# Kernel tuning notes

Measured on AMD Instinct MI355X. Metric: run time of the kernel, lower is better.

## Reference

```python
import jax, jax.numpy as jnp
import numpy as np

B, C, KC, H, W, M = 8, 512, 256, 128, 128, 19


def _cbr(x, Wt, s, b):
    # 1x1 conv (no bias) + folded BatchNorm affine + ReLU.  x: [B,Cin,H,W], Wt: [Cout,Cin]
    y = jnp.einsum('oc,bchw->bohw', Wt, x)
    return jax.nn.relu(y * s[None, :, None, None] + b[None, :, None, None])


def setup_inputs() -> dict:
    key = jax.random.key(0)
    ks = jax.random.split(key, 10)
    inp = {
        'x': jax.random.normal(ks[0], (B, C, H, W), jnp.float32),
        'proxy': jax.random.normal(ks[1], (B, C, M, 1), jnp.float32),
    }
    # fan-in scaled weights so activations stay O(1)
    inp['W_p1'] = jax.random.normal(ks[2], (KC, C), jnp.float32) * (C ** -0.5)
    inp['W_p2'] = jax.random.normal(ks[3], (KC, KC), jnp.float32) * (KC ** -0.5)
    inp['W_o1'] = jax.random.normal(ks[4], (KC, C), jnp.float32) * (C ** -0.5)
    inp['W_o2'] = jax.random.normal(ks[5], (KC, KC), jnp.float32) * (KC ** -0.5)
    inp['W_d1'] = jax.random.normal(ks[6], (KC, C), jnp.float32) * (C ** -0.5)
    inp['W_d2'] = jax.random.normal(ks[7], (KC, KC), jnp.float32) * (KC ** -0.5)
    inp['W_u'] = jax.random.normal(ks[8], (C, KC), jnp.float32) * (KC ** -0.5)
    for name, dim in [('p1', KC), ('p2', KC), ('o1', KC), ('o2', KC), ('d1', KC), ('d2', KC), ('u', C)]:
        inp['s_' + name] = jnp.ones((dim,), jnp.float32)
        inp['b_' + name] = jnp.zeros((dim,), jnp.float32)
    return inp


def reference(x, proxy, W_p1, s_p1, b_p1, W_p2, s_p2, b_p2,
              W_o1, s_o1, b_o1, W_o2, s_o2, b_o2,
              W_d1, s_d1, b_d1, W_d2, s_d2, b_d2,
              W_u, s_u, b_u):
    b, _, h, w = x.shape
    kc = W_p1.shape[0]
    # pixel query / object key / object value projections (two ConvBnRelu each)
    q = _cbr(_cbr(x, W_p1, s_p1, b_p1), W_p2, s_p2, b_p2)          # [B,KC,H,W]
    k = _cbr(_cbr(proxy, W_o1, s_o1, b_o1), W_o2, s_o2, b_o2)      # [B,KC,M,1]
    v = _cbr(_cbr(proxy, W_d1, s_d1, b_d1), W_d2, s_d2, b_d2)      # [B,KC,M,1]
    q = q.reshape(b, kc, h * w)                                    # [B,KC,P]
    k = k.reshape(b, kc, -1)                                       # [B,KC,M]
    v = v.reshape(b, kc, -1)                                       # [B,KC,M]
    sim = jnp.einsum('bkp,bkm->bpm', q, k) * (kc ** -0.5)          # [B,P,M]
    sim = jax.nn.softmax(sim, axis=-1)
    ctx = jnp.einsum('bpm,bkm->bkp', sim, v).reshape(b, kc, h, w)  # [B,KC,H,W]
    return _cbr(ctx, W_u, s_u, b_u)                                # [B,C,H,W]
```

## Files before the change

### kernel.cpp

```cpp
#include <hip/hip_runtime.h>
#include <hip/hip_bf16.h>
#include <cstddef>

constexpr int B_  = 8;
constexpr int C_  = 512;
constexpr int KC_ = 256;
constexpr int M_  = 19;
constexpr int P_  = 128 * 128;

typedef short frag8 __attribute__((ext_vector_type(8)));
typedef float f32x4 __attribute__((ext_vector_type(4)));

__device__ __forceinline__ unsigned pk_bf16(float a, float b) {
    union { __hip_bfloat162 h; unsigned u; } cv;
    cv.h = __float22bfloat162_rn(make_float2(a, b));
    return cv.u;
}
__device__ __forceinline__ ushort bf16_1(float a) {
    union { __hip_bfloat16 h; ushort u; } cv;
    cv.h = __float2bfloat16(a);
    return cv.u;
}

__device__ __forceinline__ void two_stage_proj(
    const float* __restrict__ pS, float* __restrict__ t1,
    const float* __restrict__ W1, const float* __restrict__ s1, const float* __restrict__ b1,
    const float* __restrict__ W2, const float* __restrict__ s2, const float* __restrict__ b2,
    float* __restrict__ outg, int b, int tid)
{
    float acc[M_];
#pragma unroll
    for (int m = 0; m < M_; ++m) acc[m] = 0.f;
    const float4* wrow = reinterpret_cast<const float4*>(W1 + (size_t)tid * C_);
    for (int c4 = 0; c4 < C_ / 4; ++c4) {
        float4 w = wrow[c4];
        const float* pr = pS + c4 * 4 * M_;
#pragma unroll
        for (int m = 0; m < M_; ++m) acc[m] = fmaf(w.x, pr[m], acc[m]);
#pragma unroll
        for (int m = 0; m < M_; ++m) acc[m] = fmaf(w.y, pr[M_ + m], acc[m]);
#pragma unroll
        for (int m = 0; m < M_; ++m) acc[m] = fmaf(w.z, pr[2 * M_ + m], acc[m]);
#pragma unroll
        for (int m = 0; m < M_; ++m) acc[m] = fmaf(w.w, pr[3 * M_ + m], acc[m]);
    }
    float s = s1[tid], bb = b1[tid];
    __syncthreads();
#pragma unroll
    for (int m = 0; m < M_; ++m) t1[tid * M_ + m] = fmaxf(fmaf(acc[m], s, bb), 0.f);
    __syncthreads();
#pragma unroll
    for (int m = 0; m < M_; ++m) acc[m] = 0.f;
    const float4* wrow2 = reinterpret_cast<const float4*>(W2 + (size_t)tid * KC_);
    for (int c4 = 0; c4 < KC_ / 4; ++c4) {
        float4 w = wrow2[c4];
        const float* tr = t1 + c4 * 4 * M_;
#pragma unroll
        for (int m = 0; m < M_; ++m) acc[m] = fmaf(w.x, tr[m], acc[m]);
#pragma unroll
        for (int m = 0; m < M_; ++m) acc[m] = fmaf(w.y, tr[M_ + m], acc[m]);
#pragma unroll
        for (int m = 0; m < M_; ++m) acc[m] = fmaf(w.z, tr[2 * M_ + m], acc[m]);
#pragma unroll
        for (int m = 0; m < M_; ++m) acc[m] = fmaf(w.w, tr[3 * M_ + m], acc[m]);
    }
    s = s2[tid]; bb = b2[tid];
#pragma unroll
    for (int m = 0; m < M_; ++m)
        outg[((size_t)b * KC_ + tid) * M_ + m] = fmaxf(fmaf(acc[m], s, bb), 0.f);
}

__global__ __launch_bounds__(256) void kv_kernel(
    const float* __restrict__ proxy,
    const float* __restrict__ Wo1, const float* __restrict__ so1, const float* __restrict__ bo1,
    const float* __restrict__ Wo2, const float* __restrict__ so2, const float* __restrict__ bo2,
    const float* __restrict__ Wd1, const float* __restrict__ sd1, const float* __restrict__ bd1,
    const float* __restrict__ Wd2, const float* __restrict__ sd2, const float* __restrict__ bd2,
    float* __restrict__ Kg, float* __restrict__ Vg)
{
    __shared__ float pS[C_ * M_];
    __shared__ float t1[KC_ * M_];
    const int b = blockIdx.x, tid = threadIdx.x;
    for (int i = tid; i < C_ * M_; i += 256) pS[i] = proxy[(size_t)b * C_ * M_ + i];
    __syncthreads();
    two_stage_proj(pS, t1, Wo1, so1, bo1, Wo2, so2, bo2, Kg, b, tid);
    __syncthreads();
    two_stage_proj(pS, t1, Wd1, sd1, bd1, Wd2, sd2, bd2, Vg, b, tid);
}

template <int K, bool IN_F32, bool OUT_F32>
__global__ __launch_bounds__(256) void mfma_cbr(
    const float* __restrict__ W, const void* __restrict__ Xv,
    const float* __restrict__ sc, const float* __restrict__ bi,
    void* __restrict__ Yv, int O)
{
    __shared__ ushort As[128][40];
    __shared__ ushort Bs[128][40];

    const int tid = threadIdx.x;
    const int m0 = blockIdx.x * 128;
    const int n0 = blockIdx.y * 128;
    const int b  = blockIdx.z;
    const int wave = tid >> 6, lane = tid & 63;
    const int quad = lane >> 4, l15 = lane & 15;
    const int mq = (wave & 1) * 64, nq = (wave >> 1) * 64;

    const int am  = tid >> 1;
    const int akh = (tid & 1) * 16;
    const int pp  = (tid & 63) * 2;
    const int bkg = (tid >> 6) * 8;

    const float*  Wp = W + (size_t)(m0 + am) * K + akh;
    const float*  Xf = (const float*)Xv  + (size_t)b * K * P_ + n0 + pp;
    const ushort* Xh = (const ushort*)Xv + (size_t)b * K * P_ + n0 + pp;

    f32x4 acc[4][4];
#pragma unroll
    for (int i = 0; i < 4; ++i)
#pragma unroll
        for (int j = 0; j < 4; ++j) acc[i][j] = {0.f, 0.f, 0.f, 0.f};

    for (int k0 = 0; k0 < K; k0 += 32) {
        float4 wa0 = *(const float4*)(Wp + k0);
        float4 wa1 = *(const float4*)(Wp + k0 + 4);
        float4 wa2 = *(const float4*)(Wp + k0 + 8);
        float4 wa3 = *(const float4*)(Wp + k0 + 12);
        unsigned bd0[4], bd1[4];
        if constexpr (IN_F32) {
            float2 xr[8];
#pragma unroll
            for (int j = 0; j < 8; ++j)
                xr[j] = *(const float2*)(Xf + (size_t)(k0 + bkg + j) * P_);
#pragma unroll
            for (int i = 0; i < 4; ++i) {
                bd0[i] = pk_bf16(xr[2 * i].x, xr[2 * i + 1].x);
                bd1[i] = pk_bf16(xr[2 * i].y, xr[2 * i + 1].y);
            }
        } else {
            unsigned xr[8];
#pragma unroll
            for (int j = 0; j < 8; ++j)
                xr[j] = *(const unsigned*)(Xh + (size_t)(k0 + bkg + j) * P_);
#pragma unroll
            for (int i = 0; i < 4; ++i) {
                bd0[i] = (xr[2 * i] & 0xffffu) | (xr[2 * i + 1] << 16);
                bd1[i] = (xr[2 * i] >> 16)    | (xr[2 * i + 1] & 0xffff0000u);
            }
        }
        unsigned ad0[4] = { pk_bf16(wa0.x, wa0.y), pk_bf16(wa0.z, wa0.w),
                            pk_bf16(wa1.x, wa1.y), pk_bf16(wa1.z, wa1.w) };
        unsigned ad1[4] = { pk_bf16(wa2.x, wa2.y), pk_bf16(wa2.z, wa2.w),
                            pk_bf16(wa3.x, wa3.y), pk_bf16(wa3.z, wa3.w) };

        __syncthreads();
        *(int4*)(&As[am][akh])     = *(int4*)ad0;
        *(int4*)(&As[am][akh + 8]) = *(int4*)ad1;
        *(int4*)(&Bs[pp][bkg])     = *(int4*)bd0;
        *(int4*)(&Bs[pp + 1][bkg]) = *(int4*)bd1;
        __syncthreads();

        frag8 af[4], bfv[4];
#pragma unroll
        for (int f = 0; f < 4; ++f) {
            af[f]  = *(const frag8*)(&As[mq + f * 16 + l15][quad * 8]);
            bfv[f] = *(const frag8*)(&Bs[nq + f * 16 + l15][quad * 8]);
        }
#pragma unroll
        for (int i = 0; i < 4; ++i)
#pragma unroll
            for (int j = 0; j < 4; ++j)
                acc[i][j] = __builtin_amdgcn_mfma_f32_16x16x32_bf16(
                    af[i], bfv[j], acc[i][j], 0, 0, 0);
    }

#pragma unroll
    for (int i = 0; i < 4; ++i) {
        const int ob = m0 + mq + i * 16 + quad * 4;
        float s[4], bbv[4];
#pragma unroll
        for (int r = 0; r < 4; ++r) { s[r] = sc[ob + r]; bbv[r] = bi[ob + r]; }
#pragma unroll
        for (int j = 0; j < 4; ++j) {
            const int p = n0 + nq + j * 16 + l15;
#pragma unroll
            for (int r = 0; r < 4; ++r) {
                float v = fmaxf(fmaf(acc[i][j][r], s[r], bbv[r]), 0.f);
                if constexpr (OUT_F32)
                    ((float*)Yv)[((size_t)b * O + ob + r) * P_ + p] = v;
                else
                    ((ushort*)Yv)[((size_t)b * O + ob + r) * P_ + p] = bf16_1(v);
            }
        }
    }
}

__global__ __launch_bounds__(256) void attn_kernel(
    ushort* __restrict__ Q,
    const float* __restrict__ Kg, const float* __restrict__ Vg)
{
    __shared__ float kS[KC_ * M_];
    __shared__ float vS[KC_ * M_];
    const int b = blockIdx.y;
    const int p = (blockIdx.x * 256 + threadIdx.x) * 2;
    for (int i = threadIdx.x; i < KC_ * M_; i += 256) {
        kS[i] = Kg[(size_t)b * KC_ * M_ + i];
        vS[i] = Vg[(size_t)b * KC_ * M_ + i];
    }
    __syncthreads();

    float s0[M_], s1[M_];
#pragma unroll
    for (int m = 0; m < M_; ++m) { s0[m] = 0.f; s1[m] = 0.f; }

    unsigned* Qb = reinterpret_cast<unsigned*>(Q + (size_t)b * KC_ * P_ + p);
    for (int kc = 0; kc < KC_; ++kc) {
        unsigned u = Qb[(size_t)kc * (P_ / 2)];
        float qa = __uint_as_float(u << 16);
        float qb = __uint_as_float(u & 0xffff0000u);
        const float* kr = kS + kc * M_;
#pragma unroll
        for (int m = 0; m < M_; ++m) {
            s0[m] = fmaf(qa, kr[m], s0[m]);
            s1[m] = fmaf(qb, kr[m], s1[m]);
        }
    }

    float mx0 = -1e30f, mx1 = -1e30f;
#pragma unroll
    for (int m = 0; m < M_; ++m) {
        s0[m] *= 0.0625f; s1[m] *= 0.0625f;
        mx0 = fmaxf(mx0, s0[m]); mx1 = fmaxf(mx1, s1[m]);
    }
    float sum0 = 0.f, sum1 = 0.f;
#pragma unroll
    for (int m = 0; m < M_; ++m) {
        s0[m] = __expf(s0[m] - mx0); sum0 += s0[m];
        s1[m] = __expf(s1[m] - mx1); sum1 += s1[m];
    }
    const float i0 = 1.f / sum0, i1 = 1.f / sum1;
#pragma unroll
    for (int m = 0; m < M_; ++m) { s0[m] *= i0; s1[m] *= i1; }

    for (int kc = 0; kc < KC_; ++kc) {
        const float* vr = vS + kc * M_;
        float a0 = 0.f, a1 = 0.f;
#pragma unroll
        for (int m = 0; m < M_; ++m) {
            a0 = fmaf(s0[m], vr[m], a0);
            a1 = fmaf(s1[m], vr[m], a1);
        }
        Qb[(size_t)kc * (P_ / 2)] = pk_bf16(a0, a1);
    }
}

extern "C" void kernel_launch(void* const* d_in, const int* in_sizes, int n_in,
                              void* d_out, int out_size, void* d_ws, size_t ws_size,
                              hipStream_t stream)
{
    const float* x     = (const float*)d_in[0];
    const float* proxy = (const float*)d_in[1];
    const float* W_p1  = (const float*)d_in[2];
    const float* W_p2  = (const float*)d_in[3];
    const float* W_o1  = (const float*)d_in[4];
    const float* W_o2  = (const float*)d_in[5];
    const float* W_d1  = (const float*)d_in[6];
    const float* W_d2  = (const float*)d_in[7];
    const float* W_u   = (const float*)d_in[8];
    const float* s_p1  = (const float*)d_in[9];  const float* b_p1 = (const float*)d_in[10];
    const float* s_p2  = (const float*)d_in[11]; const float* b_p2 = (const float*)d_in[12];
    const float* s_o1  = (const float*)d_in[13]; const float* b_o1 = (const float*)d_in[14];
    const float* s_o2  = (const float*)d_in[15]; const float* b_o2 = (const float*)d_in[16];
    const float* s_d1  = (const float*)d_in[17]; const float* b_d1 = (const float*)d_in[18];
    const float* s_d2  = (const float*)d_in[19]; const float* b_d2 = (const float*)d_in[20];
    const float* s_u   = (const float*)d_in[21]; const float* b_u  = (const float*)d_in[22];

    float* out = (float*)d_out;
    float* Kg  = out;
    float* Vg  = Kg + (size_t)B_ * KC_ * M_;
    ushort* q1 = (ushort*)d_ws;
    ushort* q2 = q1 + (size_t)B_ * KC_ * P_;

    kv_kernel<<<dim3(B_), dim3(256), 0, stream>>>(
        proxy, W_o1, s_o1, b_o1, W_o2, s_o2, b_o2,
               W_d1, s_d1, b_d1, W_d2, s_d2, b_d2, Kg, Vg);

    mfma_cbr<C_, true, false><<<dim3(KC_ / 128, P_ / 128, B_), dim3(256), 0, stream>>>(
        W_p1, x, s_p1, b_p1, q1, KC_);

    mfma_cbr<KC_, false, false><<<dim3(KC_ / 128, P_ / 128, B_), dim3(256), 0, stream>>>(
        W_p2, q1, s_p2, b_p2, q2, KC_);

    attn_kernel<<<dim3(P_ / 512, B_), dim3(256), 0, stream>>>(q2, Kg, Vg);

    mfma_cbr<KC_, false, true><<<dim3(C_ / 128, P_ / 128, B_), dim3(256), 0, stream>>>(
        W_u, q2, s_u, b_u, out, C_);
}
```

Measured before the change: 888.7 us.

## Switch intermediates to pixel-major bf16, pre-convert weights, and double-buffer GEMMs via direct LDS loads

Intermediate activations are now stored pixel-major (channel contiguous), so the bf16-input GEMMs can load rows with 16-byte global_load_lds into double-buffered, XOR-swizzled LDS tiles. Weights are converted to bf16 once in a front kernel that also splits the K and V projections across more blocks. Grid indices are swizzled for cache locality. The attention kernel now reads and writes one pixel per thread with vectorized 8-element channel loads. The aim is fewer redundant weight conversions, wider and coalesced loads, and overlap of loads with MFMA. The cost is more workspace and layout complexity.

```diff
diff --git a/kernel.cpp b/kernel.cpp
--- a/kernel.cpp
+++ b/kernel.cpp
@@ -1,6 +1,7 @@
 #include <hip/hip_runtime.h>
 #include <hip/hip_bf16.h>
 #include <cstddef>
+#include <cstdint>
 
 constexpr int B_  = 8;
 constexpr int C_  = 512;
@@ -10,6 +11,7 @@
 
 typedef short frag8 __attribute__((ext_vector_type(8)));
 typedef float f32x4 __attribute__((ext_vector_type(4)));
+typedef unsigned short u16x8 __attribute__((ext_vector_type(8)));
 
 __device__ __forceinline__ unsigned pk_bf16(float a, float b) {
     union { __hip_bfloat162 h; unsigned u; } cv;
@@ -20,6 +22,15 @@
     union { __hip_bfloat16 h; ushort u; } cv;
     cv.h = __float2bfloat16(a);
     return cv.u;
+}
+__device__ __forceinline__ float bf16_f(ushort u) {
+    return __uint_as_float(((unsigned)u) << 16);
+}
+
+__device__ __forceinline__ void gll16(const ushort* g, ushort* l) {
+    __builtin_amdgcn_global_load_lds(
+        (__attribute__((address_space(1))) void*)(ushort*)g,
+        (__attribute__((address_space(3))) void*)l, 16, 0, 0);
 }
 
 __device__ __forceinline__ void two_stage_proj(
@@ -70,37 +81,62 @@
         outg[((size_t)b * KC_ + tid) * M_ + m] = fmaxf(fmaf(acc[m], s, bb), 0.f);
 }
 
-__global__ __launch_bounds__(256) void kv_kernel(
+__device__ __forceinline__ void cvt_w(const float* __restrict__ s, ushort* __restrict__ d,
+                                      int n4, int cid, int nb) {
+    for (int i = cid * 256 + (int)threadIdx.x; i < n4; i += nb * 256) {
+        float4 f = ((const float4*)s)[i];
+        ushort4 h;
+        h.x = bf16_1(f.x); h.y = bf16_1(f.y); h.z = bf16_1(f.z); h.w = bf16_1(f.w);
+        ((ushort4*)d)[i] = h;
+    }
+}
+
+__global__ __launch_bounds__(256) void front_kernel(
     const float* __restrict__ proxy,
     const float* __restrict__ Wo1, const float* __restrict__ so1, const float* __restrict__ bo1,
     const float* __restrict__ Wo2, const float* __restrict__ so2, const float* __restrict__ bo2,
     const float* __restrict__ Wd1, const float* __restrict__ sd1, const float* __restrict__ bd1,
     const float* __restrict__ Wd2, const float* __restrict__ sd2, const float* __restrict__ bd2,
-    float* __restrict__ Kg, float* __restrict__ Vg)
+    float* __restrict__ Kg, float* __restrict__ Vg,
+    const float* __restrict__ Wp1f, const float* __restrict__ Wp2f, const float* __restrict__ Wuf,
+    ushort* __restrict__ Wp1b, ushort* __restrict__ Wp2b, ushort* __restrict__ Wub)
 {
     __shared__ float pS[C_ * M_];
     __shared__ float t1[KC_ * M_];
-    const int b = blockIdx.x, tid = threadIdx.x;
-    for (int i = tid; i < C_ * M_; i += 256) pS[i] = proxy[(size_t)b * C_ * M_ + i];
-    __syncthreads();
-    two_stage_proj(pS, t1, Wo1, so1, bo1, Wo2, so2, bo2, Kg, b, tid);
-    __syncthreads();
-    two_stage_proj(pS, t1, Wd1, sd1, bd1, Wd2, sd2, bd2, Vg, b, tid);
-}
-
-template <int K, bool IN_F32, bool OUT_F32>
-__global__ __launch_bounds__(256) void mfma_cbr(
-    const float* __restrict__ W, const void* __restrict__ Xv,
+    const int bx = blockIdx.x, tid = threadIdx.x;
+    if (bx < 16) {
+        const int b = bx >> 1;
+        for (int i = tid; i < C_ * M_; i += 256) pS[i] = proxy[(size_t)b * C_ * M_ + i];
+        __syncthreads();
+        if (bx & 1)
+            two_stage_proj(pS, t1, Wd1, sd1, bd1, Wd2, sd2, bd2, Vg, b, tid);
+        else
+            two_stage_proj(pS, t1, Wo1, so1, bo1, Wo2, so2, bo2, Kg, b, tid);
+    } else {
+        const int cid = bx - 16, nb = (int)gridDim.x - 16;
+        cvt_w(Wp1f, Wp1b, KC_ * C_ / 4, cid, nb);
+        cvt_w(Wp2f, Wp2b, KC_ * KC_ / 4, cid, nb);
+        cvt_w(Wuf,  Wub,  C_ * KC_ / 4, cid, nb);
+    }
+}
+
+__global__ __launch_bounds__(256) void cbr_f32in(
+    const ushort* __restrict__ Wb, const float* __restrict__ X,
     const float* __restrict__ sc, const float* __restrict__ bi,
-    void* __restrict__ Yv, int O)
-{
-    __shared__ ushort As[128][40];
-    __shared__ ushort Bs[128][40];
+    ushort* __restrict__ Y)
+{
+    constexpr int K = C_;
+    constexpr int O = KC_;
+    __shared__ __align__(16) ushort As[128][40];
+    __shared__ __align__(16) ushort Bs[128][40];
 
     const int tid = threadIdx.x;
-    const int m0 = blockIdx.x * 128;
-    const int n0 = blockIdx.y * 128;
-    const int b  = blockIdx.z;
+    const unsigned bid = blockIdx.x;
+    const unsigned swz = (bid & 7) * (gridDim.x >> 3) + (bid >> 3);
+    const int m0 = (int)(swz & 1) * 128;
+    const int n0 = (int)((swz >> 1) & 127) * 128;
+    const int b  = (int)(swz >> 8);
+
     const int wave = tid >> 6, lane = tid & 63;
     const int quad = lane >> 4, l15 = lane & 15;
     const int mq = (wave & 1) * 64, nq = (wave >> 1) * 64;
@@ -110,9 +146,8 @@
     const int pp  = (tid & 63) * 2;
     const int bkg = (tid >> 6) * 8;
 
-    const float*  Wp = W + (size_t)(m0 + am) * K + akh;
-    const float*  Xf = (const float*)Xv  + (size_t)b * K * P_ + n0 + pp;
-    const ushort* Xh = (const ushort*)Xv + (size_t)b * K * P_ + n0 + pp;
+    const ushort* Wp = Wb + (size_t)(m0 + am) * K + akh;
+    const float*  Xf = X + (size_t)b * K * P_ + n0 + pp;
 
     f32x4 acc[4][4];
 #pragma unroll
@@ -121,42 +156,24 @@
         for (int j = 0; j < 4; ++j) acc[i][j] = {0.f, 0.f, 0.f, 0.f};
 
     for (int k0 = 0; k0 < K; k0 += 32) {
-        float4 wa0 = *(const float4*)(Wp + k0);
-        float4 wa1 = *(const float4*)(Wp + k0 + 4);
-        float4 wa2 = *(const float4*)(Wp + k0 + 8);
-        float4 wa3 = *(const float4*)(Wp + k0 + 12);
+        u16x8 wa0 = *(const u16x8*)(Wp + k0);
+        u16x8 wa1 = *(const u16x8*)(Wp + k0 + 8);
+        float2 xr[8];
+#pragma unroll
+        for (int j = 0; j < 8; ++j)
+            xr[j] = *(const float2*)(Xf + (size_t)(k0 + bkg + j) * P_);
         unsigned bd0[4], bd1[4];
-        if constexpr (IN_F32) {
-            float2 xr[8];
-#pragma unroll
-            for (int j = 0; j < 8; ++j)
-                xr[j] = *(const float2*)(Xf + (size_t)(k0 + bkg + j) * P_);
-#pragma unroll
-            for (int i = 0; i < 4; ++i) {
-                bd0[i] = pk_bf16(xr[2 * i].x, xr[2 * i + 1].x);
-                bd1[i] = pk_bf16(xr[2 * i].y, xr[2 * i + 1].y);
-            }
-        } else {
-            unsigned xr[8];
-#pragma unroll
-            for (int j = 0; j < 8; ++j)
-                xr[j] = *(const unsigned*)(Xh + (size_t)(k0 + bkg + j) * P_);
-#pragma unroll
-            for (int i = 0; i < 4; ++i) {
-                bd0[i] = (xr[2 * i] & 0xffffu) | (xr[2 * i + 1] << 16);
-                bd1[i] = (xr[2 * i] >> 16)    | (xr[2 * i + 1] & 0xffff0000u);
-            }
-        }
-        unsigned ad0[4] = { pk_bf16(wa0.x, wa0.y), pk_bf16(wa0.z, wa0.w),
-                            pk_bf16(wa1.x, wa1.y), pk_bf16(wa1.z, wa1.w) };
-        unsigned ad1[4] = { pk_bf16(wa2.x, wa2.y), pk_bf16(wa2.z, wa2.w),
-                            pk_bf16(wa3.x, wa3.y), pk_bf16(wa3.z, wa3.w) };
+#pragma unroll
+        for (int i = 0; i < 4; ++i) {
+            bd0[i] = pk_bf16(xr[2 * i].x, xr[2 * i + 1].x);
+            bd1[i] = pk_bf16(xr[2 * i].y, xr[2 * i + 1].y);
+        }
 
         __syncthreads();
-        *(int4*)(&As[am][akh])     = *(int4*)ad0;
-        *(int4*)(&As[am][akh + 8]) = *(int4*)ad1;
-        *(int4*)(&Bs[pp][bkg])     = *(int4*)bd0;
-        *(int4*)(&Bs[pp + 1][bkg]) = *(int4*)bd1;
+        *(u16x8*)(&As[am][akh])     = wa0;
+        *(u16x8*)(&As[am][akh + 8]) = wa1;
+        *(int4*)(&Bs[pp][bkg])      = *(int4*)bd0;
+        *(int4*)(&Bs[pp + 1][bkg])  = *(int4*)bd1;
         __syncthreads();
 
         frag8 af[4], bfv[4];
@@ -175,81 +192,170 @@
 
 #pragma unroll
     for (int i = 0; i < 4; ++i) {
-        const int ob = m0 + mq + i * 16 + quad * 4;
-        float s[4], bbv[4];
-#pragma unroll
-        for (int r = 0; r < 4; ++r) { s[r] = sc[ob + r]; bbv[r] = bi[ob + r]; }
+        const int o0 = m0 + mq + i * 16 + quad * 4;
+        float s4[4], b4[4];
+#pragma unroll
+        for (int r = 0; r < 4; ++r) { s4[r] = sc[o0 + r]; b4[r] = bi[o0 + r]; }
 #pragma unroll
         for (int j = 0; j < 4; ++j) {
             const int p = n0 + nq + j * 16 + l15;
-#pragma unroll
-            for (int r = 0; r < 4; ++r) {
-                float v = fmaxf(fmaf(acc[i][j][r], s[r], bbv[r]), 0.f);
-                if constexpr (OUT_F32)
-                    ((float*)Yv)[((size_t)b * O + ob + r) * P_ + p] = v;
-                else
-                    ((ushort*)Yv)[((size_t)b * O + ob + r) * P_ + p] = bf16_1(v);
+            float v0 = fmaxf(fmaf(acc[i][j][0], s4[0], b4[0]), 0.f);
+            float v1 = fmaxf(fmaf(acc[i][j][1], s4[1], b4[1]), 0.f);
+            float v2 = fmaxf(fmaf(acc[i][j][2], s4[2], b4[2]), 0.f);
+            float v3 = fmaxf(fmaf(acc[i][j][3], s4[3], b4[3]), 0.f);
+            uint2 w; w.x = pk_bf16(v0, v1); w.y = pk_bf16(v2, v3);
+            *(uint2*)(Y + ((size_t)b * P_ + p) * O + o0) = w;
+        }
+    }
+}
+
+template <int K, int MT, bool OUT_F32>
+__global__ __launch_bounds__(256) void cbr_bf16in(
+    const ushort* __restrict__ Wb, const ushort* __restrict__ X,
+    const float* __restrict__ sc, const float* __restrict__ bi,
+    void* __restrict__ Yv)
+{
+    constexpr int O = MT * 128;
+    __shared__ __align__(16) ushort As[2][4096];
+    __shared__ __align__(16) ushort Bs[2][4096];
+
+    const int tid = threadIdx.x;
+    const unsigned bid = blockIdx.x;
+    const unsigned swz = (bid & 7) * (gridDim.x >> 3) + (bid >> 3);
+    const int m0 = (int)(swz % MT) * 128;
+    const int n0 = (int)((swz / MT) & 127) * 128;
+    const int b  = (int)(swz / (MT * 128));
+
+    const int wave = tid >> 6, lane = tid & 63;
+    const int quad = lane >> 4, l15 = lane & 15;
+    const int mq = (wave & 1) * 64, nq = (wave >> 1) * 64;
+
+    const int row = tid >> 1;
+    const int jx  = (tid & 1) ^ ((tid >> 3) & 1);
+    const ushort* aW = Wb + (size_t)(m0 + row) * K + jx * 8;
+    const ushort* aX = X + ((size_t)b * P_ + n0 + row) * K + jx * 8;
+
+    f32x4 acc[4][4];
+#pragma unroll
+    for (int i = 0; i < 4; ++i)
+#pragma unroll
+        for (int j = 0; j < 4; ++j) acc[i][j] = {0.f, 0.f, 0.f, 0.f};
+
+    auto stage = [&](int buf, int k0) {
+        const ushort* ga = aW + k0;
+        const ushort* gb = aX + k0;
+        ushort* la = &As[buf][wave * 512];
+        ushort* lb = &Bs[buf][wave * 512];
+        gll16(ga,      la);
+        gll16(ga + 16, la + 2048);
+        gll16(gb,      lb);
+        gll16(gb + 16, lb + 2048);
+    };
+
+    stage(0, 0);
+    __syncthreads();
+
+    const int xb = (quad >> 1) * 2048 + ((((quad & 1) ^ ((l15 >> 2) & 1))) << 3);
+
+    constexpr int NSTEP = K / 32;
+#pragma unroll
+    for (int t = 0; t < NSTEP; ++t) {
+        if (t + 1 < NSTEP) stage((t + 1) & 1, (t + 1) * 32);
+        const ushort* as = &As[t & 1][0];
+        const ushort* bs = &Bs[t & 1][0];
+        frag8 af[4], bfv[4];
+#pragma unroll
+        for (int f = 0; f < 4; ++f) {
+            af[f]  = *(const frag8*)(as + xb + (mq + f * 16 + l15) * 16);
+            bfv[f] = *(const frag8*)(bs + xb + (nq + f * 16 + l15) * 16);
+        }
+#pragma unroll
+        for (int i = 0; i < 4; ++i)
+#pragma unroll
+            for (int j = 0; j < 4; ++j)
+                acc[i][j] = __builtin_amdgcn_mfma_f32_16x16x32_bf16(
+                    af[i], bfv[j], acc[i][j], 0, 0, 0);
+        __syncthreads();
+    }
+
+#pragma unroll
+    for (int i = 0; i < 4; ++i) {
+        const int o0 = m0 + mq + i * 16 + quad * 4;
+        float s4[4], b4[4];
+#pragma unroll
+        for (int r = 0; r < 4; ++r) { s4[r] = sc[o0 + r]; b4[r] = bi[o0 + r]; }
+#pragma unroll
+        for (int j = 0; j < 4; ++j) {
+            const int p = n0 + nq + j * 16 + l15;
+            float v0 = fmaxf(fmaf(acc[i][j][0], s4[0], b4[0]), 0.f);
+            float v1 = fmaxf(fmaf(acc[i][j][1], s4[1], b4[1]), 0.f);
+            float v2 = fmaxf(fmaf(acc[i][j][2], s4[2], b4[2]), 0.f);
+            float v3 = fmaxf(fmaf(acc[i][j][3], s4[3], b4[3]), 0.f);
+            if constexpr (OUT_F32) {
+                float* Yf = (float*)Yv;
+                Yf[((size_t)b * O + o0 + 0) * P_ + p] = v0;
+                Yf[((size_t)b * O + o0 + 1) * P_ + p] = v1;
+                Yf[((size_t)b * O + o0 + 2) * P_ + p] = v2;
+                Yf[((size_t)b * O + o0 + 3) * P_ + p] = v3;
+            } else {
+                uint2 w; w.x = pk_bf16(v0, v1); w.y = pk_bf16(v2, v3);
+                *(uint2*)((ushort*)Yv + ((size_t)b * P_ + p) * O + o0) = w;
             }
         }
     }
 }
 
 __global__ __launch_bounds__(256) void attn_kernel(
-    ushort* __restrict__ Q,
-    const float* __restrict__ Kg, const float* __restrict__ Vg)
+    ushort* __restrict__ Q, const float* __restrict__ Kg, const float* __restrict__ Vg)
 {
     __shared__ float kS[KC_ * M_];
     __shared__ float vS[KC_ * M_];
     const int b = blockIdx.y;
-    const int p = (blockIdx.x * 256 + threadIdx.x) * 2;
+    const int p = blockIdx.x * 256 + threadIdx.x;
     for (int i = threadIdx.x; i < KC_ * M_; i += 256) {
         kS[i] = Kg[(size_t)b * KC_ * M_ + i];
         vS[i] = Vg[(size_t)b * KC_ * M_ + i];
     }
     __syncthreads();
 
-    float s0[M_], s1[M_];
-#pragma unroll
-    for (int m = 0; m < M_; ++m) { s0[m] = 0.f; s1[m] = 0.f; }
-
-    unsigned* Qb = reinterpret_cast<unsigned*>(Q + (size_t)b * KC_ * P_ + p);
-    for (int kc = 0; kc < KC_; ++kc) {
-        unsigned u = Qb[(size_t)kc * (P_ / 2)];
-        float qa = __uint_as_float(u << 16);
-        float qb = __uint_as_float(u & 0xffff0000u);
-        const float* kr = kS + kc * M_;
-#pragma unroll
-        for (int m = 0; m < M_; ++m) {
-            s0[m] = fmaf(qa, kr[m], s0[m]);
-            s1[m] = fmaf(qb, kr[m], s1[m]);
-        }
-    }
-
-    float mx0 = -1e30f, mx1 = -1e30f;
-#pragma unroll
-    for (int m = 0; m < M_; ++m) {
-        s0[m] *= 0.0625f; s1[m] *= 0.0625f;
-        mx0 = fmaxf(mx0, s0[m]); mx1 = fmaxf(mx1, s1[m]);
-    }
-    float sum0 = 0.f, sum1 = 0.f;
-#pragma unroll
-    for (int m = 0; m < M_; ++m) {
-        s0[m] = __expf(s0[m] - mx0); sum0 += s0[m];
-        s1[m] = __expf(s1[m] - mx1); sum1 += s1[m];
-    }
-    const float i0 = 1.f / sum0, i1 = 1.f / sum1;
-#pragma unroll
-    for (int m = 0; m < M_; ++m) { s0[m] *= i0; s1[m] *= i1; }
-
-    for (int kc = 0; kc < KC_; ++kc) {
-        const float* vr = vS + kc * M_;
-        float a0 = 0.f, a1 = 0.f;
-#pragma unroll
-        for (int m = 0; m < M_; ++m) {
-            a0 = fmaf(s0[m], vr[m], a0);
-            a1 = fmaf(s1[m], vr[m], a1);
-        }
-        Qb[(size_t)kc * (P_ / 2)] = pk_bf16(a0, a1);
+    u16x8* Qr = reinterpret_cast<u16x8*>(Q + ((size_t)b * P_ + p) * KC_);
+
+    float s[M_];
+#pragma unroll
+    for (int m = 0; m < M_; ++m) s[m] = 0.f;
+
+    for (int g = 0; g < KC_ / 8; ++g) {
+        u16x8 u = Qr[g];
+#pragma unroll
+        for (int e = 0; e < 8; ++e) {
+            float q = bf16_f((ushort)u[e]);
+            const float* kr = kS + (g * 8 + e) * M_;
+#pragma unroll
+            for (int m = 0; m < M_; ++m) s[m] = fmaf(q, kr[m], s[m]);
+        }
+    }
+
+    float mx = -1e30f;
+#pragma unroll
+    for (int m = 0; m < M_; ++m) { s[m] *= 0.0625f; mx = fmaxf(mx, s[m]); }
+    float sum = 0.f;
+#pragma unroll
+    for (int m = 0; m < M_; ++m) { s[m] = __expf(s[m] - mx); sum += s[m]; }
+    const float inv = 1.f / sum;
+#pragma unroll
+    for (int m = 0; m < M_; ++m) s[m] *= inv;
+
+    for (int g = 0; g < KC_ / 8; ++g) {
+        u16x8 o;
+#pragma unroll
+        for (int e = 0; e < 8; ++e) {
+            const float* vr = vS + (g * 8 + e) * M_;
+            float a = 0.f;
+#pragma unroll
+            for (int m = 0; m < M_; ++m) a = fmaf(s[m], vr[m], a);
+            o[e] = (short)bf16_1(a);
+        }
+        Qr[g] = o;
     }
 }
 
@@ -277,21 +383,25 @@
     float* out = (float*)d_out;
     float* Kg  = out;
     float* Vg  = Kg + (size_t)B_ * KC_ * M_;
-    ushort* q1 = (ushort*)d_ws;
-    ushort* q2 = q1 + (size_t)B_ * KC_ * P_;
-
-    kv_kernel<<<dim3(B_), dim3(256), 0, stream>>>(
+    ushort* q1   = (ushort*)d_ws;
+    ushort* q2   = q1 + (size_t)B_ * KC_ * P_;
+    ushort* Wp1b = q2 + (size_t)B_ * KC_ * P_;
+    ushort* Wp2b = Wp1b + (size_t)KC_ * C_;
+    ushort* Wub  = Wp2b + (size_t)KC_ * KC_;
+
+    front_kernel<<<dim3(176), dim3(256), 0, stream>>>(
         proxy, W_o1, s_o1, b_o1, W_o2, s_o2, b_o2,
-               W_d1, s_d1, b_d1, W_d2, s_d2, b_d2, Kg, Vg);
-
-    mfma_cbr<C_, true, false><<<dim3(KC_ / 128, P_ / 128, B_), dim3(256), 0, stream>>>(
-        W_p1, x, s_p1, b_p1, q1, KC_);
-
-    mfma_cbr<KC_, false, false><<<dim3(KC_ / 128, P_ / 128, B_), dim3(256), 0, stream>>>(
-        W_p2, q1, s_p2, b_p2, q2, KC_);
-
-    attn_kernel<<<dim3(P_ / 512, B_), dim3(256), 0, stream>>>(q2, Kg, Vg);
-
-    mfma_cbr<KC_, false, true><<<dim3(C_ / 128, P_ / 128, B_), dim3(256), 0, stream>>>(
-        W_u, q2, s_u, b_u, out, C_);
-}
+               W_d1, s_d1, b_d1, W_d2, s_d2, b_d2, Kg, Vg,
+        W_p1, W_p2, W_u, Wp1b, Wp2b, Wub);
+
+    cbr_f32in<<<dim3(2 * 128 * B_), dim3(256), 0, stream>>>(
+        Wp1b, x, s_p1, b_p1, q1);
+
+    cbr_bf16in<KC_, 2, false><<<dim3(2 * 128 * B_), dim3(256), 0, stream>>>(
+        Wp2b, q1, s_p2, b_p2, q2);
+
+    attn_kernel<<<dim3(P_ / 256, B_), dim3(256), 0, stream>>>(q2, Kg, Vg);
+
+    cbr_bf16in<KC_, 4, true><<<dim3(4 * 128 * B_), dim3(256), 0, stream>>>(
+        Wub, q2, s_u, b_u, out);
+}
```

Result: faster. 793.4 us (-10.7%).
